# Performance work log

Measured on AMD Instinct MI355X. Metric: run time of the kernel, lower is better.

## Reference

```python
import jax, jax.numpy as jnp
import numpy as np

B, S, E, H, FF = 2, 2048, 768, 12, 3072
D = E // H
EPS = 1e-5


def setup_inputs() -> dict:
    key = jax.random.key(0)
    ks = jax.random.split(key, 12)
    sc = lambda n: 1.0 / np.sqrt(n)
    return {
        "x": jax.random.normal(ks[0], (B, S, E), jnp.float32),
        "wq": jax.random.normal(ks[1], (E, E), jnp.float32) * sc(E),
        "wk": jax.random.normal(ks[2], (E, E), jnp.float32) * sc(E),
        "wv": jax.random.normal(ks[3], (E, E), jnp.float32) * sc(E),
        "wo": jax.random.normal(ks[4], (E, E), jnp.float32) * sc(E),
        "bo": jax.random.normal(ks[5], (E,), jnp.float32) * 0.02,
        "w1": jax.random.normal(ks[6], (FF, E), jnp.float32) * sc(E),
        "b1": jax.random.normal(ks[7], (FF,), jnp.float32) * 0.02,
        "w2": jax.random.normal(ks[8], (E, FF), jnp.float32) * sc(FF),
        "b2": jax.random.normal(ks[9], (E,), jnp.float32) * 0.02,
        "gamma": jnp.ones((E,), jnp.float32),
        "beta": jnp.zeros((E,), jnp.float32),
    }


def _layernorm(x, g, b):
    mu = jnp.mean(x, axis=-1, keepdims=True)
    var = jnp.mean(jnp.square(x - mu), axis=-1, keepdims=True)
    return (x - mu) * jax.lax.rsqrt(var + EPS) * g + b


def reference(x, wq, wk, wv, wo, bo, w1, b1, w2, b2, gamma, beta):
    res = x
    xn = _layernorm(x, gamma, beta)
    # Q/K/V projections (torch Linear: y = x @ W.T), split into heads
    q = (xn @ wq.T).reshape(B, S, H, D)
    k = (xn @ wk.T).reshape(B, S, H, D)
    v = (xn @ wv.T).reshape(B, S, H, D)
    scale = jnp.sqrt(jnp.float32(D))
    scores = jnp.einsum("bqhd,bkhd->bhqk", q, k) / scale  # [B,H,S,S]
    causal = jnp.tril(jnp.ones((S, S), bool))
    scores = jnp.where(causal, scores, -jnp.inf)
    w = jax.nn.softmax(scores, axis=-1)
    attn = jnp.einsum("bhqk,bkhd->bqhd", w, v).reshape(B, S, E)
    attn = attn @ wo.T + bo
    res = res + attn
    y = _layernorm(res, gamma, beta)  # NOTE: same LayerNorm params reused (as in source)
    h = jax.nn.gelu(y @ w1.T + b1, approximate=False)  # nn.GELU default is exact erf
    ffn = h @ w2.T + b2
    return res + ffn
```

## Files before the change

kernel.cpp:

```cpp
#include <hip/hip_runtime.h>
#include <hip/hip_bf16.h>
#include <math.h>

typedef __bf16 bf16_8 __attribute__((ext_vector_type(8)));
typedef __bf16 bf16_4 __attribute__((ext_vector_type(4)));
typedef float f32x4 __attribute__((ext_vector_type(4)));

#define AS1 __attribute__((address_space(1)))
#define AS3 __attribute__((address_space(3)))

__global__ __launch_bounds__(256) void ln_kernel(
    const float* __restrict__ x, const float* __restrict__ g,
    const float* __restrict__ b, __hip_bfloat16* __restrict__ out, int cols) {
  const int row = blockIdx.x;
  const int t = threadIdx.x;
  float loc[3];
  float s = 0.f, s2 = 0.f;
#pragma unroll
  for (int i = 0; i < 3; ++i) {
    float v = x[(size_t)row * cols + t + i * 256];
    loc[i] = v;
    s += v;
    s2 += v * v;
  }
#pragma unroll
  for (int off = 32; off; off >>= 1) {
    s += __shfl_down(s, off);
    s2 += __shfl_down(s2, off);
  }
  __shared__ float red[2][4];
  const int lane = t & 63, w = t >> 6;
  if (lane == 0) {
    red[0][w] = s;
    red[1][w] = s2;
  }
  __syncthreads();
  s = red[0][0] + red[0][1] + red[0][2] + red[0][3];
  s2 = red[1][0] + red[1][1] + red[1][2] + red[1][3];
  const float mu = s / cols;
  const float var = s2 / cols - mu * mu;
  const float rs = rsqrtf(var + 1e-5f);
  __hip_bfloat16* orow = out + (size_t)row * cols;
#pragma unroll
  for (int i = 0; i < 3; ++i) {
    int c = t + i * 256;
    orow[c] = __hip_bfloat16((loc[i] - mu) * rs * g[c] + b[c]);
  }
}

__global__ __launch_bounds__(256) void reduce_ln(
    const float* __restrict__ x, const float* __restrict__ part, int nz,
    const float* __restrict__ bias, const float* __restrict__ g,
    const float* __restrict__ b, float* __restrict__ res,
    __hip_bfloat16* __restrict__ yout) {
  const int row = blockIdx.x;
  const int t = threadIdx.x;
  const size_t zstride = (size_t)4096 * 768;
  float loc[3];
  float s = 0.f, s2 = 0.f;
#pragma unroll
  for (int i = 0; i < 3; ++i) {
    const int c = t + i * 256;
    const size_t off = (size_t)row * 768 + c;
    float v = x[off] + bias[c];
    for (int z = 0; z < nz; ++z) v += part[(size_t)z * zstride + off];
    res[off] = v;
    loc[i] = v;
    s += v;
    s2 += v * v;
  }
#pragma unroll
  for (int off = 32; off; off >>= 1) {
    s += __shfl_down(s, off);
    s2 += __shfl_down(s2, off);
  }
  __shared__ float red[2][4];
  const int lane = t & 63, w = t >> 6;
  if (lane == 0) {
    red[0][w] = s;
    red[1][w] = s2;
  }
  __syncthreads();
  s = red[0][0] + red[0][1] + red[0][2] + red[0][3];
  s2 = red[1][0] + red[1][1] + red[1][2] + red[1][3];
  const float mu = s / 768.f;
  const float var = s2 / 768.f - mu * mu;
  const float rs = rsqrtf(var + 1e-5f);
#pragma unroll
  for (int i = 0; i < 3; ++i) {
    const int c = t + i * 256;
    yout[(size_t)row * 768 + c] = __hip_bfloat16((loc[i] - mu) * rs * g[c] + b[c]);
  }
}

__global__ __launch_bounds__(256) void reduce_out(
    const float* __restrict__ part, int nz, const float* __restrict__ bias,
    float* __restrict__ res) {
  const int row = blockIdx.x;
  const int t = threadIdx.x;
  const size_t zstride = (size_t)4096 * 768;
#pragma unroll
  for (int i = 0; i < 3; ++i) {
    const int c = t + i * 256;
    const size_t off = (size_t)row * 768 + c;
    float v = res[off] + bias[c];
    for (int z = 0; z < nz; ++z) v += part[(size_t)z * zstride + off];
    res[off] = v;
  }
}

__global__ __launch_bounds__(256) void cvt_multi(
    const float* __restrict__ sa, const float* __restrict__ sb,
    const float* __restrict__ sc, const float* __restrict__ sd,
    __hip_bfloat16* __restrict__ da, __hip_bfloat16* __restrict__ db,
    __hip_bfloat16* __restrict__ dc, __hip_bfloat16* __restrict__ dd) {
  const float* src;
  __hip_bfloat16* dst;
  if (blockIdx.y == 0) { src = sa; dst = da; }
  else if (blockIdx.y == 1) { src = sb; dst = db; }
  else if (blockIdx.y == 2) { src = sc; dst = dc; }
  else { src = sd; dst = dd; }
  const size_t i = ((size_t)blockIdx.x * 256 + threadIdx.x) * 4;
  float4 f = *(const float4*)(src + i);
  bf16_4 o;
  o[0] = (__bf16)f.x; o[1] = (__bf16)f.y; o[2] = (__bf16)f.z; o[3] = (__bf16)f.w;
  *(bf16_4*)((__bf16*)dst + i) = o;
}

__global__ __launch_bounds__(256) void transpose_v(
    const __hip_bfloat16* __restrict__ v, __hip_bfloat16* __restrict__ vt) {
  const int S = 2048, E = 768, H = 12;
  const int s0 = blockIdx.x * 64;
  const int bh = blockIdx.y;
  const int b = bh / H, h = bh - b * H;
  __shared__ __align__(16) __bf16 T[64 * 72];
  const int tid = threadIdx.x;
#pragma unroll
  for (int u = 0; u < 2; ++u) {
    int i = tid + u * 256;
    int sr = i >> 3, c = i & 7;
    *(bf16_8*)(&T[sr * 72 + c * 8]) =
        *(const bf16_8*)(v + ((size_t)b * S + s0 + sr) * E + h * 64 + c * 8);
  }
  __syncthreads();
#pragma unroll
  for (int u = 0; u < 2; ++u) {
    int i = tid + u * 256;
    int dr = i >> 3, kc = i & 7;
    bf16_8 o;
#pragma unroll
    for (int e = 0; e < 8; ++e) {
      int k = 32 * (kc >> 2) + 16 * (e >> 2) + 4 * (kc & 3) + (e & 3);
      o[e] = T[k * 72 + dr];
    }
    *(bf16_8*)(vt + ((size_t)bh * 64 + dr) * S + s0 + kc * 8) = o;
  }
}

template <int MODE, bool BF32>
__global__ __launch_bounds__(256) void gemm_bt(
    const __hip_bfloat16* __restrict__ A, const void* __restrict__ Bx,
    const float* __restrict__ bias, void* __restrict__ out,
    int M, int N, int K, int lda, int ldb, int ldout) {
  constexpr int BM = 128, BN = 128, BK = 64;
  constexpr int LDBP = BF32 ? 72 : BK;
  __shared__ __align__(16) __bf16 As[BM * BK];
  __shared__ __align__(16) __bf16 Bs[BN * LDBP];
  const int tid = threadIdx.x;
  const int m0 = blockIdx.y * BM;
  const int n0 = blockIdx.x * BN;
  const int wave = tid >> 6;
  const int lane = tid & 63;
  const int quad = lane >> 4;
  const int l16 = lane & 15;
  const int wm = (wave & 1) * 64;
  const int wn = (wave >> 1) * 64;

  int kbase = 0, kcnt = K;
  if constexpr (MODE == 2 || MODE == 3) {
    kcnt = K / gridDim.z;
    kbase = blockIdx.z * kcnt;
  }

  const int srow = lane >> 3;
  const int scol = ((lane & 7) ^ (srow & 7)) * 8;
  const __hip_bfloat16* Ap = A + (size_t)(m0 + wave * 8 + srow) * lda + kbase + scol;
  const __hip_bfloat16* Bpb = nullptr;
  const float* Bpf = nullptr;
  if constexpr (BF32)
    Bpf = (const float*)Bx;
  else
    Bpb = (const __hip_bfloat16*)Bx + (size_t)(n0 + wave * 8 + srow) * ldb + kbase + scol;

  f32x4 acc[4][4] = {};

  for (int k0 = 0; k0 < kcnt; k0 += BK) {
    __syncthreads();
#pragma unroll
    for (int u = 0; u < 4; ++u) {
      __builtin_amdgcn_global_load_lds(
          (const AS1 void*)(Ap + (size_t)(u * 32) * lda + k0),
          (AS3 void*)(&As[(u * 32 + wave * 8) * BK]), 16, 0, 0);
      if constexpr (!BF32)
        __builtin_amdgcn_global_load_lds(
            (const AS1 void*)(Bpb + (size_t)(u * 32) * ldb + k0),
            (AS3 void*)(&Bs[(u * 32 + wave * 8) * BK]), 16, 0, 0);
    }
    if constexpr (BF32) {
#pragma unroll
      for (int u = 0; u < 4; ++u) {
        int c = u * 256 + tid;
        int row = c >> 3, kc = c & 7;
        const float* src = Bpf + (size_t)(n0 + row) * ldb + kbase + k0 + kc * 8;
        float4 f0 = *(const float4*)src;
        float4 f1 = *(const float4*)(src + 4);
        bf16_8 bv;
        bv[0] = (__bf16)f0.x; bv[1] = (__bf16)f0.y; bv[2] = (__bf16)f0.z; bv[3] = (__bf16)f0.w;
        bv[4] = (__bf16)f1.x; bv[5] = (__bf16)f1.y; bv[6] = (__bf16)f1.z; bv[7] = (__bf16)f1.w;
        *(bf16_8*)(&Bs[row * LDBP + kc * 8]) = bv;
      }
    }
    __syncthreads();
#pragma unroll
    for (int kk = 0; kk < 2; ++kk) {
      bf16_8 af[4], bfr[4];
#pragma unroll
      for (int i = 0; i < 4; ++i)
        af[i] = *(const bf16_8*)(
            &As[(wm + i * 16 + l16) * BK + (((kk * 4 + quad) ^ (l16 & 7)) * 8)]);
#pragma unroll
      for (int j = 0; j < 4; ++j) {
        if constexpr (BF32)
          bfr[j] = *(const bf16_8*)(&Bs[(wn + j * 16 + l16) * LDBP + kk * 32 + quad * 8]);
        else
          bfr[j] = *(const bf16_8*)(
              &Bs[(wn + j * 16 + l16) * BK + (((kk * 4 + quad) ^ (l16 & 7)) * 8)]);
      }
#pragma unroll
      for (int i = 0; i < 4; ++i)
#pragma unroll
        for (int j = 0; j < 4; ++j)
          acc[i][j] =
              __builtin_amdgcn_mfma_f32_16x16x32_bf16(af[i], bfr[j], acc[i][j], 0, 0, 0);
    }
  }

#pragma unroll
  for (int i = 0; i < 4; ++i) {
#pragma unroll
    for (int j = 0; j < 4; ++j) {
#pragma unroll
      for (int r = 0; r < 4; ++r) {
        const int row = m0 + wm + i * 16 + quad * 4 + r;
        const int col = n0 + wn + j * 16 + l16;
        const float v = acc[i][j][r];
        if constexpr (MODE == 0) {
          const int tsel = n0 / 768;
          const size_t idx = ((size_t)tsel * M + row) * 768 + (col - tsel * 768);
          ((__hip_bfloat16*)out)[idx] = __hip_bfloat16(v);
        } else if constexpr (MODE == 1) {
          float tt = v + bias[col];
          float gl = 0.5f * tt * (1.0f + erff(tt * 0.70710678118654752f));
          ((__hip_bfloat16*)out)[(size_t)row * ldout + col] = __hip_bfloat16(gl);
        } else if constexpr (MODE == 2) {
          float add = v + ((blockIdx.z == 0 && bias) ? bias[col] : 0.f);
          atomicAdd((float*)out + (size_t)row * 768 + col, add);
        } else {
          ((float*)out)[(size_t)blockIdx.z * M * 768 + (size_t)row * 768 + col] = v;
        }
      }
    }
  }
}

__global__ void zero_ctr(int* __restrict__ c) {
  if (threadIdx.x == 0) *c = 0;
}

#define ALDP 72
__device__ __constant__ signed char UQ[48] = {
    31, 31, 30, 15, 30, 29, 29, 28, 14, 28, 27, 27, 26, 13, 26, 25,
    25, 24, 12, 24, 23, 23, 22, 11, 22, 21, 21, 20, 10, 20, 19, 19,
    18, 9, 18, 17, 17, 16, 8, 16, 7, 6, 5, 4, 3, 2, 1, 0};
__device__ __constant__ signed char UP[48] = {
    0, 1, 1, 2, 0, 0, 1, 1, 2, 0, 0, 1, 1, 2, 0, 0,
    1, 1, 2, 0, 0, 1, 1, 2, 0, 0, 1, 1, 2, 0, 0, 1,
    1, 2, 0, 0, 1, 1, 2, 0, 2, 2, 2, 2, 2, 2, 2, 2};

template <bool PRE_T, bool SPLIT>
__global__ __launch_bounds__(256) void attn_mfma(
    const __hip_bfloat16* __restrict__ qb, const __hip_bfloat16* __restrict__ kb,
    const __hip_bfloat16* __restrict__ vb, __hip_bfloat16* __restrict__ ob,
    float* __restrict__ po, float* __restrict__ pml, int* __restrict__ ctr) {
  const int S = 2048, H = 12, E = 768;
  const int tid = threadIdx.x;
  const int wave = tid >> 6;
  const int lane = tid & 63;
  const int quad = lane >> 4;
  const int l16 = lane & 15;

  __shared__ __align__(16) __bf16 Ks[2][64 * 64];
  __shared__ __align__(16) __bf16 Vt[2][64 * 64];
  __shared__ int task;
  __bf16* ep = &Ks[0][0] + wave * 16 * ALDP;

  const int srow8 = lane >> 3;
  const int csrc = ((lane & 7) ^ srow8) * 8;
  const float SCL = 0.18033688011112042f;
  const int NTASK = SPLIT ? 24 * 48 : 24 * 32;

  for (;;) {
    if (tid == 0) task = atomicAdd(ctr, 1);
    __syncthreads();
    const int t = task;
    if (t >= NTASK) return;
    int qblk, part, bh;
    if constexpr (SPLIT) {
      const int unit = t / 24;
      bh = t - unit * 24;
      qblk = UQ[unit];
      part = UP[unit];
    } else {
      qblk = 31 - (t / 24);
      bh = t - (t / 24) * 24;
      part = 2;
    }
    const int b = bh / H, h = bh - b * H;
    const int q0 = qblk * 64;
    const int qw = q0 + wave * 16;
    const size_t base = (size_t)b * S * E + (size_t)h * 64;
    const int mid = (qblk + 1) >> 1;
    const int kbgn = (part == 1) ? mid : 0;
    const int kend = (part == 0) ? mid : qblk + 1;

    auto STAGE = [&](int kts, int buf) {
      const int k0s = kts * 64;
#pragma unroll
      for (int u = 0; u < 2; ++u) {
        const int trow = wave * 16 + u * 8;
        __builtin_amdgcn_global_load_lds(
            (const AS1 void*)(kb + base + (size_t)(k0s + trow + srow8) * E + csrc),
            (AS3 void*)(&Ks[buf][trow * 64]), 16, 0, 0);
        if constexpr (PRE_T)
          __builtin_amdgcn_global_load_lds(
              (const AS1 void*)(vb + ((size_t)(bh * 64 + trow + srow8)) * S + k0s + csrc),
              (AS3 void*)(&Vt[buf][trow * 64]), 16, 0, 0);
      }
      if constexpr (!PRE_T) {
#pragma unroll
        for (int u = 0; u < 2; ++u) {
          int i = tid + u * 256;
          int kr = i & 63, dq = i >> 6;
          bf16_8 vv = *(const bf16_8*)(vb + base + (size_t)(k0s + kr) * E + dq * 8);
          const int c = 32 * (kr >> 5) + 8 * ((kr >> 2) & 3) + 4 * ((kr >> 4) & 1) + (kr & 3);
#pragma unroll
          for (int j = 0; j < 8; ++j) {
            int drow = dq * 8 + j;
            Vt[buf][drow * 64 + (((c >> 3) ^ (drow & 7)) * 8) + (c & 7)] = vv[j];
          }
        }
      }
    };

    bf16_8 qf[2];
#pragma unroll
    for (int s = 0; s < 2; ++s)
      qf[s] = *(const bf16_8*)(qb + base + (size_t)(qw + l16) * E + s * 32 + quad * 8);

    f32x4 o[4] = {};
    float mq = -1e30f, lq = 0.f;

    STAGE(kbgn, 0);
    __syncthreads();
    int cur = 0;

    for (int kt = kbgn; kt < kend; ++kt) {
      const int k0 = kt * 64;
      if (kt + 1 < kend) STAGE(kt + 1, cur ^ 1);

      f32x4 sc[4] = {};
      __builtin_amdgcn_s_setprio(1);
#pragma unroll
      for (int jj = 0; jj < 4; ++jj)
#pragma unroll
        for (int s = 0; s < 2; ++s) {
          bf16_8 kf = *(const bf16_8*)(
              &Ks[cur][(jj * 16 + l16) * 64 + (((s * 4 + quad) ^ (l16 & 7)) * 8)]);
          sc[jj] = __builtin_amdgcn_mfma_f32_16x16x32_bf16(kf, qf[s], sc[jj], 0, 0, 0);
        }
      __builtin_amdgcn_s_setprio(0);

#pragma unroll
      for (int jj = 0; jj < 4; ++jj)
#pragma unroll
        for (int r = 0; r < 4; ++r) sc[jj][r] *= SCL;
      if (kt == qblk) {
#pragma unroll
        for (int jj = 0; jj < 4; ++jj)
#pragma unroll
          for (int r = 0; r < 4; ++r)
            if ((k0 + jj * 16 + quad * 4 + r) > (qw + l16)) sc[jj][r] = -1e30f;
      }
      float mj[4];
#pragma unroll
      for (int jj = 0; jj < 4; ++jj)
        mj[jj] = fmaxf(fmaxf(sc[jj][0], sc[jj][1]), fmaxf(sc[jj][2], sc[jj][3]));
      float mx = fmaxf(fmaxf(mj[0], mj[1]), fmaxf(mj[2], mj[3]));
      mx = fmaxf(mx, __shfl_xor(mx, 16));
      mx = fmaxf(mx, __shfl_xor(mx, 32));
      const float mn = fmaxf(mq, mx);
      const float corr = exp2f(mq - mn);
      mq = mn;
      float sj[4];
#pragma unroll
      for (int jj = 0; jj < 4; ++jj) {
#pragma unroll
        for (int r = 0; r < 4; ++r) sc[jj][r] = exp2f(sc[jj][r] - mn);
        sj[jj] = (sc[jj][0] + sc[jj][1]) + (sc[jj][2] + sc[jj][3]);
      }
      float sum = (sj[0] + sj[1]) + (sj[2] + sj[3]);
      sum += __shfl_xor(sum, 16);
      sum += __shfl_xor(sum, 32);
      lq = lq * corr + sum;
#pragma unroll
      for (int nt2 = 0; nt2 < 4; ++nt2)
#pragma unroll
        for (int r = 0; r < 4; ++r) o[nt2][r] *= corr;

      bf16_8 pf[2];
#pragma unroll
      for (int s = 0; s < 2; ++s)
#pragma unroll
        for (int r = 0; r < 4; ++r) {
          pf[s][r] = (__bf16)sc[2 * s][r];
          pf[s][4 + r] = (__bf16)sc[2 * s + 1][r];
        }

      __builtin_amdgcn_s_setprio(1);
#pragma unroll
      for (int s = 0; s < 2; ++s)
#pragma unroll
        for (int dt = 0; dt < 4; ++dt) {
          bf16_8 vf = *(const bf16_8*)(
              &Vt[cur][(dt * 16 + l16) * 64 + (((s * 4 + quad) ^ (l16 & 7)) * 8)]);
          o[dt] = __builtin_amdgcn_mfma_f32_16x16x32_bf16(vf, pf[s], o[dt], 0, 0, 0);
        }
      __builtin_amdgcn_s_setprio(0);

      __syncthreads();
      cur ^= 1;
    }

    if (SPLIT && part != 2) {
      const int cidx = bh * 16 + (qblk - 16);
      float* poT = po + (size_t)cidx * 8192 + part * 4096;
      const int ql = wave * 16 + l16;
#pragma unroll
      for (int dt = 0; dt < 4; ++dt)
#pragma unroll
        for (int r = 0; r < 4; ++r)
          poT[(dt * 16 + quad * 4 + r) * 64 + ql] = o[dt][r];
      if (quad == 0) {
        pml[(size_t)cidx * 256 + part * 128 + ql] = mq;
        pml[(size_t)cidx * 256 + part * 128 + 64 + ql] = lq;
      }
    } else {
      const float inv = 1.f / lq;
#pragma unroll
      for (int dt = 0; dt < 4; ++dt) {
        bf16_4 o4;
#pragma unroll
        for (int r = 0; r < 4; ++r) o4[r] = (__bf16)(o[dt][r] * inv);
        *(bf16_4*)(&ep[l16 * ALDP + dt * 16 + quad * 4]) = o4;
      }
#pragma unroll
      for (int u = 0; u < 2; ++u) {
        int j = lane + u * 64;
        int ql = j >> 3, ch = j & 7;
        bf16_8 ov = *(const bf16_8*)(&ep[ql * ALDP + ch * 8]);
        *(bf16_8*)(ob + base + (size_t)(qw + ql) * E + ch * 8) = ov;
      }
    }
  }
}

__global__ __launch_bounds__(256) void attn_combine(
    const float* __restrict__ po, const float* __restrict__ pml,
    __hip_bfloat16* __restrict__ ob) {
  const int S = 2048, H = 12, E = 768;
  const int cidx = blockIdx.x;
  const int bh = cidx / 16;
  const int qblk = 16 + (cidx - bh * 16);
  const int b = bh / H, h = bh - b * H;
  const int q0 = qblk * 64;
  const size_t base = (size_t)b * S * E + (size_t)h * 64;
  const float* P0 = po + (size_t)cidx * 8192;
  const float* P1 = P0 + 4096;
  const float* ML = pml + (size_t)cidx * 256;

  __shared__ float a1[64], a2[64], dn[64];
  const int t = threadIdx.x;
  if (t < 64) {
    const float m1 = ML[t], l1 = ML[64 + t];
    const float m2 = ML[128 + t], l2 = ML[192 + t];
    const float ms = fmaxf(m1, m2);
    const float e1 = exp2f(m1 - ms), e2 = exp2f(m2 - ms);
    a1[t] = e1;
    a2[t] = e2;
    dn[t] = 1.f / (e1 * l1 + e2 * l2);
  }
  __syncthreads();
  const int d = t & 63;
  const int qg = t >> 6;
#pragma unroll
  for (int i = 0; i < 16; ++i) {
    const int q = qg + i * 4;
    const float v = (a1[q] * P0[d * 64 + q] + a2[q] * P1[d * 64 + q]) * dn[q];
    ob[base + (size_t)(q0 + q) * E + d] = __hip_bfloat16(v);
  }
}

extern "C" void kernel_launch(void* const* d_in, const int* in_sizes, int n_in,
                              void* d_out, int out_size, void* d_ws, size_t ws_size,
                              hipStream_t stream) {
  const int Bv = 2, S = 2048, E = 768, FF = 3072;
  const int M = Bv * S;
  const size_t ME = (size_t)M * E;
  const size_t EE = (size_t)E * E;
  const size_t EF = (size_t)E * FF;

  const float* x = (const float*)d_in[0];
  const float* wq = (const float*)d_in[1];
  const float* wk = (const float*)d_in[2];
  const float* wv = (const float*)d_in[3];
  const float* wo = (const float*)d_in[4];
  const float* bo = (const float*)d_in[5];
  const float* w1 = (const float*)d_in[6];
  const float* b1 = (const float*)d_in[7];
  const float* w2 = (const float*)d_in[8];
  const float* b2 = (const float*)d_in[9];
  const float* gamma = (const float*)d_in[10];
  const float* beta = (const float*)d_in[11];

  int* ctr = (int*)d_ws;
  __hip_bfloat16* slot = (__hip_bfloat16*)((char*)d_ws + 256);
  __hip_bfloat16* s0 = slot;
  __hip_bfloat16* s1 = slot + ME;
  __hip_bfloat16* s4 = slot + 4 * ME;
  __hip_bfloat16* s5 = slot + 5 * ME;
  float* pp = (float*)(slot + 5 * ME + 2 * EF);
  __hip_bfloat16* vt = (__hip_bfloat16*)pp;
  float* po = (float*)((char*)pp + ME * sizeof(__hip_bfloat16));
  float* pml = po + (size_t)384 * 8192;
  float* res = (float*)d_out;

  const size_t need_mid = 256 + (5 * ME + 2 * EF) * sizeof(__hip_bfloat16);
  const size_t need_full = need_mid + 4 * ME * sizeof(float);
  const bool full = ws_size >= need_full;
  const bool mid = ws_size >= need_mid;

  cvt_multi<<<dim3(EE / 1024, 4), 256, 0, stream>>>(
      wq, wk, wv, wo, s4, s4 + EE, s4 + 2 * EE, s4 + 3 * EE);
  if (mid)
    cvt_multi<<<dim3(EF / 1024, 2), 256, 0, stream>>>(
        w1, w2, nullptr, nullptr, s5, s5 + EF, nullptr, nullptr);
  ln_kernel<<<M, 256, 0, stream>>>(x, gamma, beta, s0, E);
  gemm_bt<0, false><<<dim3(18, 32), 256, 0, stream>>>(s0, s4, nullptr, s1, M, 2304, E, E, E, 0);
  zero_ctr<<<1, 64, 0, stream>>>(ctr);
  if (full) {
    transpose_v<<<dim3(32, 24), 256, 0, stream>>>(s1 + 2 * ME, vt);
    attn_mfma<true, true><<<1024, 256, 0, stream>>>(s1, s1 + ME, vt, s0, po, pml, ctr);
    attn_combine<<<384, 256, 0, stream>>>(po, pml, s0);
  } else {
    attn_mfma<false, false><<<768, 256, 0, stream>>>(
        s1, s1 + ME, s1 + 2 * ME, s0, nullptr, nullptr, ctr);
  }

  if (full) {
    gemm_bt<3, false><<<dim3(6, 32, 4), 256, 0, stream>>>(
        s0, s4 + 3 * EE, nullptr, pp, M, E, E, E, E, 0);
    reduce_ln<<<M, 256, 0, stream>>>(x, pp, 4, bo, gamma, beta, res, s0);
    gemm_bt<1, false><<<dim3(24, 32), 256, 0, stream>>>(s0, s5, b1, s1, M, FF, E, E, E, FF);
    gemm_bt<3, false><<<dim3(6, 32, 4), 256, 0, stream>>>(
        s1, s5 + EF, nullptr, pp, M, E, FF, FF, FF, 0);
    reduce_out<<<M, 256, 0, stream>>>(pp, 4, b2, res);
  } else {
    hipMemcpyAsync(d_out, x, ME * sizeof(float), hipMemcpyDeviceToDevice, stream);
    gemm_bt<2, false><<<dim3(6, 32, 2), 256, 0, stream>>>(
        s0, s4 + 3 * EE, bo, res, M, E, E, E, E, 0);
    ln_kernel<<<M, 256, 0, stream>>>(res, gamma, beta, s0, E);
    if (mid) {
      gemm_bt<1, false><<<dim3(24, 32), 256, 0, stream>>>(s0, s5, b1, s1, M, FF, E, E, E, FF);
      gemm_bt<2, false><<<dim3(6, 32, 4), 256, 0, stream>>>(
          s1, s5 + EF, b2, res, M, E, FF, FF, FF, 0);
    } else {
      gemm_bt<1, true><<<dim3(24, 32), 256, 0, stream>>>(s0, w1, b1, s1, M, FF, E, E, E, FF);
      cvt_multi<<<dim3(EF / 1024, 1), 256, 0, stream>>>(
          w2, nullptr, nullptr, nullptr, s0, nullptr, nullptr, nullptr);
      gemm_bt<2, false><<<dim3(6, 32, 4), 256, 0, stream>>>(
          s1, s0, b2, res, M, E, FF, FF, FF, 0);
    }
  }
}
```

Measured before the change: 328.7 us.

## Single-buffer K tile in attention, transpose combine output via LDS, raise grid size

The attention kernel drops K from double to single buffering. The prefetch of the next K/V tiles now starts after a barrier that follows the QK MFMAs, so K's LDS footprint halves and more blocks may fit per CU. The combine kernel writes through a padded LDS transpose so output rows are stored as coalesced 16-byte bf16 vectors instead of strided scalar stores. The persistent attention grid grows from 1024 to 1152 blocks, matching the task count, at the cost of an extra barrier per key tile and a shorter prefetch window for K.

```diff
diff --git a/kernel.cpp b/kernel.cpp
--- a/kernel.cpp
+++ b/kernel.cpp
@@ -299,10 +299,10 @@
   const int quad = lane >> 4;
   const int l16 = lane & 15;
 
-  __shared__ __align__(16) __bf16 Ks[2][64 * 64];
+  __shared__ __align__(16) __bf16 Ks[64 * 64];
   __shared__ __align__(16) __bf16 Vt[2][64 * 64];
   __shared__ int task;
-  __bf16* ep = &Ks[0][0] + wave * 16 * ALDP;
+  __bf16* ep = &Vt[0][0] + wave * 16 * ALDP;
 
   const int srow8 = lane >> 3;
   const int csrc = ((lane & 7) ^ srow8) * 8;
@@ -333,20 +333,27 @@
     const int kbgn = (part == 1) ? mid : 0;
     const int kend = (part == 0) ? mid : qblk + 1;
 
-    auto STAGE = [&](int kts, int buf) {
+    auto STAGE_K = [&](int kts) {
       const int k0s = kts * 64;
 #pragma unroll
       for (int u = 0; u < 2; ++u) {
         const int trow = wave * 16 + u * 8;
         __builtin_amdgcn_global_load_lds(
             (const AS1 void*)(kb + base + (size_t)(k0s + trow + srow8) * E + csrc),
-            (AS3 void*)(&Ks[buf][trow * 64]), 16, 0, 0);
-        if constexpr (PRE_T)
+            (AS3 void*)(&Ks[trow * 64]), 16, 0, 0);
+      }
+    };
+    auto STAGE_V = [&](int kts, int buf) {
+      const int k0s = kts * 64;
+      if constexpr (PRE_T) {
+#pragma unroll
+        for (int u = 0; u < 2; ++u) {
+          const int trow = wave * 16 + u * 8;
           __builtin_amdgcn_global_load_lds(
               (const AS1 void*)(vb + ((size_t)(bh * 64 + trow + srow8)) * S + k0s + csrc),
               (AS3 void*)(&Vt[buf][trow * 64]), 16, 0, 0);
-      }
-      if constexpr (!PRE_T) {
+        }
+      } else {
 #pragma unroll
         for (int u = 0; u < 2; ++u) {
           int i = tid + u * 256;
@@ -370,13 +377,13 @@
     f32x4 o[4] = {};
     float mq = -1e30f, lq = 0.f;
 
-    STAGE(kbgn, 0);
+    STAGE_K(kbgn);
+    STAGE_V(kbgn, 0);
     __syncthreads();
     int cur = 0;
 
     for (int kt = kbgn; kt < kend; ++kt) {
       const int k0 = kt * 64;
-      if (kt + 1 < kend) STAGE(kt + 1, cur ^ 1);
 
       f32x4 sc[4] = {};
       __builtin_amdgcn_s_setprio(1);
@@ -385,10 +392,16 @@
 #pragma unroll
         for (int s = 0; s < 2; ++s) {
           bf16_8 kf = *(const bf16_8*)(
-              &Ks[cur][(jj * 16 + l16) * 64 + (((s * 4 + quad) ^ (l16 & 7)) * 8)]);
+              &Ks[(jj * 16 + l16) * 64 + (((s * 4 + quad) ^ (l16 & 7)) * 8)]);
           sc[jj] = __builtin_amdgcn_mfma_f32_16x16x32_bf16(kf, qf[s], sc[jj], 0, 0, 0);
         }
       __builtin_amdgcn_s_setprio(0);
+
+      __syncthreads();
+      if (kt + 1 < kend) {
+        STAGE_K(kt + 1);
+        STAGE_V(kt + 1, cur ^ 1);
+      }
 
 #pragma unroll
       for (int jj = 0; jj < 4; ++jj)
@@ -489,8 +502,8 @@
     __hip_bfloat16* __restrict__ ob) {
   const int S = 2048, H = 12, E = 768;
   const int cidx = blockIdx.x;
-  const int bh = cidx / 16;
-  const int qblk = 16 + (cidx - bh * 16);
+  const int bh = cidx >> 4;
+  const int qblk = 16 + (cidx & 15);
   const int b = bh / H, h = bh - b * H;
   const int q0 = qblk * 64;
   const size_t base = (size_t)b * S * E + (size_t)h * 64;
@@ -499,6 +512,7 @@
   const float* ML = pml + (size_t)cidx * 256;
 
   __shared__ float a1[64], a2[64], dn[64];
+  __shared__ float T[64 * 65];
   const int t = threadIdx.x;
   if (t < 64) {
     const float m1 = ML[t], l1 = ML[64 + t];
@@ -510,13 +524,23 @@
     dn[t] = 1.f / (e1 * l1 + e2 * l2);
   }
   __syncthreads();
-  const int d = t & 63;
-  const int qg = t >> 6;
+  const int q = t & 63;
+  const int w = t >> 6;
 #pragma unroll
   for (int i = 0; i < 16; ++i) {
-    const int q = qg + i * 4;
-    const float v = (a1[q] * P0[d * 64 + q] + a2[q] * P1[d * 64 + q]) * dn[q];
-    ob[base + (size_t)(q0 + q) * E + d] = __hip_bfloat16(v);
+    const int d = w * 16 + i;
+    T[q * 65 + d] = (a1[q] * P0[d * 64 + q] + a2[q] * P1[d * 64 + q]) * dn[q];
+  }
+  __syncthreads();
+  const int c8 = t & 7;
+  const int qr = t >> 3;
+#pragma unroll
+  for (int p = 0; p < 2; ++p) {
+    const int qq = qr + p * 32;
+    bf16_8 ov;
+#pragma unroll
+    for (int j = 0; j < 8; ++j) ov[j] = (__bf16)T[qq * 65 + c8 * 8 + j];
+    *(bf16_8*)(ob + base + (size_t)(q0 + qq) * E + c8 * 8) = ov;
   }
 }
 
@@ -569,7 +593,7 @@
   zero_ctr<<<1, 64, 0, stream>>>(ctr);
   if (full) {
     transpose_v<<<dim3(32, 24), 256, 0, stream>>>(s1 + 2 * ME, vt);
-    attn_mfma<true, true><<<1024, 256, 0, stream>>>(s1, s1 + ME, vt, s0, po, pml, ctr);
+    attn_mfma<true, true><<<1152, 256, 0, stream>>>(s1, s1 + ME, vt, s0, po, pml, ctr);
     attn_combine<<<384, 256, 0, stream>>>(po, pml, s0);
   } else {
     attn_mfma<false, false><<<768, 256, 0, stream>>>(
```

New measurement: 317.6 us. -3.4%, faster.
